# Kernel tuning notes

Measured on AMD Instinct MI355X. Metric: run time of the kernel, lower is better.

## Reference

```python
import jax, jax.numpy as jnp
import numpy as np

B, T, V, H = 128, 256, 512, 1024
EOS_ID = 1


def _onehot_seq(key, eos_pos):
    k1, = jax.random.split(key, 1)
    toks = jax.random.randint(k1, (B, T), 2, V)  # avoid 0/1 so EOS only where planted
    toks = toks.at[jnp.arange(B), eos_pos].set(EOS_ID)
    return jax.nn.one_hot(toks, V, dtype=jnp.float32)


def setup_inputs() -> dict:
    key = jax.random.key(0)
    ks = jax.random.split(key, 12)
    enc_eos = jax.random.randint(ks[0], (B,), T // 2, T)
    dec_eos = jax.random.randint(ks[1], (B,), T // 2, T)
    s = 0.05
    return {
        "encoder_inputs": _onehot_seq(ks[2], enc_eos),
        "decoder_inputs": _onehot_seq(ks[3], dec_eos),
        "enc_Wi": jax.random.normal(ks[4], (V, 4 * H), jnp.float32) * s,
        "enc_Wh": jax.random.normal(ks[5], (H, 4 * H), jnp.float32) * s,
        "enc_b": jnp.zeros((4 * H,), jnp.float32),
        "dec_Wi": jax.random.normal(ks[6], (V, 4 * H), jnp.float32) * s,
        "dec_Wh": jax.random.normal(ks[7], (H, 4 * H), jnp.float32) * s,
        "dec_b": jnp.zeros((4 * H,), jnp.float32),
        "dense_W": jax.random.normal(ks[8], (H, V), jnp.float32) * s,
        "dense_b": jnp.zeros((V,), jnp.float32),
    }


def get_sequence_lengths(seq, eos_id=EOS_ID):
    eos_row = seq[:, :, eos_id]                      # [B,T]
    eos_idx = jnp.argmax(eos_row == eos_id, axis=-1)  # first position hitting EOS
    found = eos_row[jnp.arange(seq.shape[0]), eos_idx] == eos_id
    return jnp.where(found, eos_idx + 1, seq.shape[1])


def lstm_scan(c0, h0, x_btv, Wi, Wh, b):
    """Scans an LSTM over time axis 1; returns (c_seq, h_seq) each [B,T,H]."""
    def step(carry, x):
        c, h = carry
        z = x @ Wi + h @ Wh + b                      # [B,4H]
        i, f, g, o = jnp.split(z, 4, axis=-1)
        c = jax.nn.sigmoid(f) * c + jax.nn.sigmoid(i) * jnp.tanh(g)
        h = jax.nn.sigmoid(o) * jnp.tanh(c)
        return (c, h), (c, h)
    xs = jnp.swapaxes(x_btv, 0, 1)                   # [T,B,V]
    _, (cs, hs) = jax.lax.scan(step, (c0, h0), xs)
    return jnp.swapaxes(cs, 0, 1), jnp.swapaxes(hs, 0, 1)


def reference(encoder_inputs, decoder_inputs, enc_Wi, enc_Wh, enc_b,
              dec_Wi, dec_Wh, dec_b, dense_W, dense_b):
    b = encoder_inputs.shape[0]
    # --- encoder ---
    lengths = get_sequence_lengths(encoder_inputs)
    idx = jnp.maximum(0, lengths - 1)
    c0 = jnp.zeros((b, H), encoder_inputs.dtype)
    h0 = jnp.zeros((b, H), encoder_inputs.dtype)
    cs, hs = lstm_scan(c0, h0, encoder_inputs, enc_Wi, enc_Wh, enc_b)
    ar = jnp.arange(b)
    c_enc, h_enc = cs[ar, idx], hs[ar, idx]          # carry at EOS step
    # --- decoder (teacher forcing on decoder_inputs[:, :-1]) ---
    _, hd = lstm_scan(c_enc, h_enc, decoder_inputs[:, :-1], dec_Wi, dec_Wh, dec_b)
    logits = hd @ dense_W + dense_b                  # [B,T-1,V]
    return logits
```

## Files before the change

kernel.cpp:

```cpp
#include <hip/hip_runtime.h>

#define Bv 128
#define Tv 256
#define Vv 512
#define Hv 1024
#define FH 4096
#define TD 255

typedef unsigned short ushort_t;
typedef __attribute__((ext_vector_type(8))) short bf16x8;
typedef __attribute__((ext_vector_type(4))) float f32x4;

__device__ __forceinline__ ushort_t f2bf(float f) {
    unsigned u = __float_as_uint(f);
    unsigned r = (u + 0x7fffu + ((u >> 16) & 1u)) >> 16;
    return (ushort_t)r;
}
__device__ __forceinline__ float bf2f(ushort_t h) {
    return __uint_as_float(((unsigned)h) << 16);
}
__device__ __forceinline__ float sigm(float x) {
    return 1.0f / (1.0f + expf(-x));
}

__global__ __launch_bounds__(256) void wsplit_t(
    const float* __restrict__ W, int K, int N,
    ushort_t* __restrict__ hiT, ushort_t* __restrict__ loT)
{
    __shared__ float ts[32][65];
    const int n0 = blockIdx.x * 64, k0 = blockIdx.y * 32;
    const int tid = threadIdx.x;
#pragma unroll
    for (int i = 0; i < 8; i++) {
        int f = tid + i * 256;
        int k = f >> 6, nn = f & 63;
        ts[k][nn] = W[(size_t)(k0 + k) * N + n0 + nn];
    }
    __syncthreads();
#pragma unroll
    for (int i = 0; i < 8; i++) {
        int f = tid + i * 256;
        int nn = f >> 5, k = f & 31;
        float v = ts[k][nn];
        ushort_t h = f2bf(v);
        ushort_t l = f2bf(v - bf2f(h));
        size_t o = (size_t)(n0 + nn) * K + k0 + k;
        hiT[o] = h;
        loT[o] = l;
    }
}

__global__ __launch_bounds__(256) void extract_tokens(
    const float* __restrict__ x, int* __restrict__ tok)
{
    int row = blockIdx.x * 4 + (threadIdx.x >> 6);
    int lane = threadIdx.x & 63;
    const float* p = x + (size_t)row * Vv;
    int found = -1;
#pragma unroll
    for (int i = 0; i < 8; i++)
        if (p[lane + i * 64] > 0.5f) found = lane + i * 64;
#pragma unroll
    for (int off = 32; off > 0; off >>= 1) {
        int o = __shfl_down(found, off);
        found = found > o ? found : o;
    }
    if (lane == 0) tok[row] = found;
}

__global__ void find_eos(const int* __restrict__ tok, int* __restrict__ idx)
{
    int b = threadIdx.x;
    int first = Tv - 1;
    for (int t = Tv - 1; t >= 0; t--)
        if (tok[b * Tv + t] == 1) first = t;
    idx[b] = first;
}

__global__ __launch_bounds__(256) void lstm_step(
    const ushort_t* __restrict__ WhiT, const ushort_t* __restrict__ WloT,
    const float* __restrict__ Wi,
    const float* __restrict__ bias,
    const int* __restrict__ tok, int t,
    const ushort_t* __restrict__ hin_hi, const ushort_t* __restrict__ hin_lo,
    ushort_t* __restrict__ hout_hi, ushort_t* __restrict__ hout_lo,
    float* __restrict__ c_state,
    ushort_t* __restrict__ hex_hi, ushort_t* __restrict__ hex_lo,
    const int* __restrict__ save_idx,
    float* __restrict__ c_save, ushort_t* __restrict__ hs_hi, ushort_t* __restrict__ hs_lo)
{
    __shared__ float z_s[32][68];
    const int tid = threadIdx.x;
    const int wave = tid >> 6, lane = tid & 63;
    const int wm = wave & 1, wn = wave >> 1;
    const int n = lane & 15, quad = lane >> 4;
    const int j0 = blockIdx.x * 16;
    const int b0 = blockIdx.y * 32;

    const size_t arow = (size_t)(b0 + wm * 16 + n) * Hv + quad * 8;
    const size_t g0 = (size_t)((2 * wn + 0) * Hv + j0 + n) * Hv + quad * 8;
    const size_t g1 = (size_t)((2 * wn + 1) * Hv + j0 + n) * Hv + quad * 8;

    f32x4 acc0 = {0.f, 0.f, 0.f, 0.f}, acc1 = {0.f, 0.f, 0.f, 0.f};

#pragma unroll 2
    for (int kc = 0; kc < Hv; kc += 32) {
        bf16x8 ahi = *(const bf16x8*)(hin_hi + arow + kc);
        bf16x8 alo = *(const bf16x8*)(hin_lo + arow + kc);
        bf16x8 b0h = *(const bf16x8*)(WhiT + g0 + kc);
        bf16x8 b0l = *(const bf16x8*)(WloT + g0 + kc);
        bf16x8 b1h = *(const bf16x8*)(WhiT + g1 + kc);
        bf16x8 b1l = *(const bf16x8*)(WloT + g1 + kc);
        acc0 = __builtin_amdgcn_mfma_f32_16x16x32_bf16(ahi, b0h, acc0, 0, 0, 0);
        acc1 = __builtin_amdgcn_mfma_f32_16x16x32_bf16(ahi, b1h, acc1, 0, 0, 0);
        acc0 = __builtin_amdgcn_mfma_f32_16x16x32_bf16(alo, b0h, acc0, 0, 0, 0);
        acc1 = __builtin_amdgcn_mfma_f32_16x16x32_bf16(alo, b1h, acc1, 0, 0, 0);
        acc0 = __builtin_amdgcn_mfma_f32_16x16x32_bf16(ahi, b0l, acc0, 0, 0, 0);
        acc1 = __builtin_amdgcn_mfma_f32_16x16x32_bf16(ahi, b1l, acc1, 0, 0, 0);
    }

    const int row0 = wm * 16 + quad * 4;
    const int cb0 = (2 * wn + 0) * 16 + n;
    const int cb1 = cb0 + 16;
#pragma unroll
    for (int r = 0; r < 4; r++) {
        z_s[row0 + r][cb0] = acc0[r];
        z_s[row0 + r][cb1] = acc1[r];
    }
    __syncthreads();

#pragma unroll
    for (int i = 0; i < 2; i++) {
        int p = tid + i * 256;
        int bl = p >> 4, jl = p & 15;
        int b = b0 + bl, col = j0 + jl;
        int tk = tok[b * Tv + t];
        const float* wr = Wi + (size_t)tk * FH + col;
        float zi = z_s[bl][jl]      + wr[0]        + bias[col];
        float zf = z_s[bl][16 + jl] + wr[Hv]       + bias[Hv + col];
        float zg = z_s[bl][32 + jl] + wr[2 * Hv]   + bias[2 * Hv + col];
        float zo = z_s[bl][48 + jl] + wr[3 * Hv]   + bias[3 * Hv + col];
        float si = sigm(zi), sf = sigm(zf), so = sigm(zo);
        float gg = tanhf(zg);
        size_t off = (size_t)b * Hv + col;
        float cn = sf * c_state[off] + si * gg;
        float hn = so * tanhf(cn);
        c_state[off] = cn;
        ushort_t hh = f2bf(hn);
        ushort_t hl = f2bf(hn - bf2f(hh));
        hout_hi[off] = hh;
        hout_lo[off] = hl;
        if (hex_hi) { hex_hi[off] = hh; hex_lo[off] = hl; }
        if (save_idx) {
            if (t == save_idx[b]) { c_save[off] = cn; hs_hi[off] = hh; hs_lo[off] = hl; }
        }
    }
}

__global__ __launch_bounds__(256) void dense_mfma(
    const ushort_t* __restrict__ Ahi, const ushort_t* __restrict__ Alo,
    const ushort_t* __restrict__ WhiT, const ushort_t* __restrict__ WloT,
    const float* __restrict__ bias, float* __restrict__ out)
{
    const int tid = threadIdx.x;
    const int wave = tid >> 6, lane = tid & 63;
    const int wm = wave & 1, wn = wave >> 1;
    const int n = lane & 15, quad = lane >> 4;
    const int m0 = blockIdx.y * 32 + wm * 16;
    const int c0 = blockIdx.x * 64 + wn * 32;

    const size_t arow = (size_t)(m0 + n) * Hv + quad * 8;
    const size_t g0 = (size_t)(c0 + 0 + n) * Hv + quad * 8;
    const size_t g1 = (size_t)(c0 + 16 + n) * Hv + quad * 8;

    f32x4 acc0 = {0.f, 0.f, 0.f, 0.f}, acc1 = {0.f, 0.f, 0.f, 0.f};

#pragma unroll 2
    for (int kc = 0; kc < Hv; kc += 32) {
        bf16x8 ahi = *(const bf16x8*)(Ahi + arow + kc);
        bf16x8 alo = *(const bf16x8*)(Alo + arow + kc);
        bf16x8 b0h = *(const bf16x8*)(WhiT + g0 + kc);
        bf16x8 b0l = *(const bf16x8*)(WloT + g0 + kc);
        bf16x8 b1h = *(const bf16x8*)(WhiT + g1 + kc);
        bf16x8 b1l = *(const bf16x8*)(WloT + g1 + kc);
        acc0 = __builtin_amdgcn_mfma_f32_16x16x32_bf16(ahi, b0h, acc0, 0, 0, 0);
        acc1 = __builtin_amdgcn_mfma_f32_16x16x32_bf16(ahi, b1h, acc1, 0, 0, 0);
        acc0 = __builtin_amdgcn_mfma_f32_16x16x32_bf16(alo, b0h, acc0, 0, 0, 0);
        acc1 = __builtin_amdgcn_mfma_f32_16x16x32_bf16(alo, b1h, acc1, 0, 0, 0);
        acc0 = __builtin_amdgcn_mfma_f32_16x16x32_bf16(ahi, b0l, acc0, 0, 0, 0);
        acc1 = __builtin_amdgcn_mfma_f32_16x16x32_bf16(ahi, b1l, acc1, 0, 0, 0);
    }

#pragma unroll
    for (int r = 0; r < 4; r++) {
        int row = m0 + quad * 4 + r;
        int tt = row >> 7, bb = row & 127;
        size_t o = ((size_t)bb * TD + tt) * Vv;
        int col0 = c0 + n, col1 = c0 + 16 + n;
        out[o + col0] = acc0[r] + bias[col0];
        out[o + col1] = acc1[r] + bias[col1];
    }
}

extern "C" void kernel_launch(void* const* d_in, const int* in_sizes, int n_in,
                              void* d_out, int out_size, void* d_ws, size_t ws_size,
                              hipStream_t stream)
{
    const float* enc_in  = (const float*)d_in[0];
    const float* dec_in  = (const float*)d_in[1];
    const float* enc_Wi  = (const float*)d_in[2];
    const float* enc_Wh  = (const float*)d_in[3];
    const float* enc_b   = (const float*)d_in[4];
    const float* dec_Wi  = (const float*)d_in[5];
    const float* dec_Wh  = (const float*)d_in[6];
    const float* dec_b   = (const float*)d_in[7];
    const float* dense_W = (const float*)d_in[8];
    const float* dense_b = (const float*)d_in[9];
    float* out = (float*)d_out;

    char* wp = (char*)d_ws;
    auto take = [&](size_t bytes) -> char* {
        char* p = wp;
        wp += (bytes + 255) & ~(size_t)255;
        return p;
    };

    ushort_t* hd_hi = (ushort_t*)take((size_t)TD * Bv * Hv * 2);
    ushort_t* hd_lo = (ushort_t*)take((size_t)TD * Bv * Hv * 2);
    ushort_t* eWhi  = (ushort_t*)take((size_t)FH * Hv * 2);
    ushort_t* eWlo  = (ushort_t*)take((size_t)FH * Hv * 2);
    ushort_t* dWhi  = (ushort_t*)take((size_t)FH * Hv * 2);
    ushort_t* dWlo  = (ushort_t*)take((size_t)FH * Hv * 2);
    ushort_t* nWhi  = (ushort_t*)take((size_t)Vv * Hv * 2);
    ushort_t* nWlo  = (ushort_t*)take((size_t)Vv * Hv * 2);
    ushort_t* hbh0  = (ushort_t*)take((size_t)Bv * Hv * 2);
    ushort_t* hbl0  = (ushort_t*)take((size_t)Bv * Hv * 2);
    ushort_t* hbh1  = (ushort_t*)take((size_t)Bv * Hv * 2);
    ushort_t* hbl1  = (ushort_t*)take((size_t)Bv * Hv * 2);
    ushort_t* hshi  = (ushort_t*)take((size_t)Bv * Hv * 2);
    ushort_t* hslo  = (ushort_t*)take((size_t)Bv * Hv * 2);
    float*    c_state = (float*)take((size_t)Bv * Hv * 4);
    float*    c_save  = (float*)take((size_t)Bv * Hv * 4);
    int*      etok  = (int*)take((size_t)Bv * Tv * 4);
    int*      dtok  = (int*)take((size_t)Bv * Tv * 4);
    int*      eidx  = (int*)take((size_t)Bv * 4);

    ushort_t* hbh[2] = {hbh0, hbh1};
    ushort_t* hbl[2] = {hbl0, hbl1};

    wsplit_t<<<dim3(FH / 64, Hv / 32), 256, 0, stream>>>(enc_Wh, Hv, FH, eWhi, eWlo);
    wsplit_t<<<dim3(FH / 64, Hv / 32), 256, 0, stream>>>(dec_Wh, Hv, FH, dWhi, dWlo);
    wsplit_t<<<dim3(Vv / 64, Hv / 32), 256, 0, stream>>>(dense_W, Hv, Vv, nWhi, nWlo);
    extract_tokens<<<Bv * Tv / 4, 256, 0, stream>>>(enc_in, etok);
    extract_tokens<<<Bv * Tv / 4, 256, 0, stream>>>(dec_in, dtok);
    find_eos<<<1, Bv, 0, stream>>>(etok, eidx);

    hipMemsetAsync(hbh0, 0, (size_t)Bv * Hv * 2, stream);
    hipMemsetAsync(hbl0, 0, (size_t)Bv * Hv * 2, stream);
    hipMemsetAsync(c_state, 0, (size_t)Bv * Hv * 4, stream);

    for (int t = 0; t < Tv; t++) {
        lstm_step<<<dim3(64, 4), 256, 0, stream>>>(
            eWhi, eWlo, enc_Wi, enc_b, etok, t,
            hbh[t & 1], hbl[t & 1], hbh[(t + 1) & 1], hbl[(t + 1) & 1],
            c_state, nullptr, nullptr, eidx, c_save, hshi, hslo);
    }

    hipMemcpyAsync(c_state, c_save, (size_t)Bv * Hv * 4, hipMemcpyDeviceToDevice, stream);
    hipMemcpyAsync(hbh0, hshi, (size_t)Bv * Hv * 2, hipMemcpyDeviceToDevice, stream);
    hipMemcpyAsync(hbl0, hslo, (size_t)Bv * Hv * 2, hipMemcpyDeviceToDevice, stream);

    for (int t = 0; t < TD; t++) {
        lstm_step<<<dim3(64, 4), 256, 0, stream>>>(
            dWhi, dWlo, dec_Wi, dec_b, dtok, t,
            hbh[t & 1], hbl[t & 1], hbh[(t + 1) & 1], hbl[(t + 1) & 1],
            c_state, hd_hi + (size_t)t * Bv * Hv, hd_lo + (size_t)t * Bv * Hv,
            nullptr, nullptr, nullptr, nullptr);
    }

    dense_mfma<<<dim3(Vv / 64, (TD * Bv) / 32), 256, 0, stream>>>(
        hd_hi, hd_lo, nWhi, nWlo, dense_b, out);
}
```

Baseline: 14.29 ms.

## Replace per-step LSTM launches with persistent cooperative kernel holding Wh in LDS

The 511 separate per-timestep lstm_step launches are replaced by one cooperative persistent kernel of 256 blocks. Each block keeps its 32-row slice of the recurrent weights (hi/lo bf16) resident in shared memory, keeps the cell state in registers, and separates timesteps with a grid-wide barrier. This removes per-step launch overhead and the repeated global reads of the 32 MB split weight matrices each step, and it drops the c_state round trips and device-to-device copies between encoder and decoder. In exchange every step pays a grid.sync. The kernel also depends on all 256 blocks with about 130 KB of LDS each being co-resident, which is needed for the cooperative launch to succeed.

```diff
diff --git a/kernel.cpp b/kernel.cpp
--- a/kernel.cpp
+++ b/kernel.cpp
@@ -1,4 +1,7 @@
 #include <hip/hip_runtime.h>
+#include <hip/hip_cooperative_groups.h>
+
+namespace cg = cooperative_groups;
 
 #define Bv 128
 #define Tv 256
@@ -6,6 +9,10 @@
 #define Hv 1024
 #define FH 4096
 #define TD 255
+
+#define WSTRIDE 1032
+#define W_ELEMS (32 * WSTRIDE)
+#define SMEM_BYTES (2 * W_ELEMS * 2 + 64 * 33 * 4)
 
 typedef unsigned short ushort_t;
 typedef __attribute__((ext_vector_type(8))) short bf16x8;
@@ -77,82 +84,127 @@
     idx[b] = first;
 }
 
-__global__ __launch_bounds__(256) void lstm_step(
-    const ushort_t* __restrict__ WhiT, const ushort_t* __restrict__ WloT,
-    const float* __restrict__ Wi,
-    const float* __restrict__ bias,
-    const int* __restrict__ tok, int t,
-    const ushort_t* __restrict__ hin_hi, const ushort_t* __restrict__ hin_lo,
-    ushort_t* __restrict__ hout_hi, ushort_t* __restrict__ hout_lo,
-    float* __restrict__ c_state,
-    ushort_t* __restrict__ hex_hi, ushort_t* __restrict__ hex_lo,
-    const int* __restrict__ save_idx,
-    float* __restrict__ c_save, ushort_t* __restrict__ hs_hi, ushort_t* __restrict__ hs_lo)
-{
-    __shared__ float z_s[32][68];
+struct PParams {
+    const ushort_t *eWhi, *eWlo, *dWhi, *dWlo;
+    const float *Wi_e, *b_e, *Wi_d, *b_d;
+    const int *etok, *dtok, *eidx;
+    ushort_t *h0h, *h0l, *h1h, *h1l;
+    ushort_t *hdh, *hdl;
+};
+
+__device__ __forceinline__ void load_wlds(
+    ushort_t* dst_hi, ushort_t* dst_lo,
+    const ushort_t* __restrict__ Whi, const ushort_t* __restrict__ Wlo, int j0)
+{
+    const int c = threadIdx.x >> 4, seg = threadIdx.x & 15;
+    const int grow = (c >> 3) * Hv + j0 + (c & 7);
+    const ushort_t* sh = Whi + (size_t)grow * Hv + seg * 64;
+    const ushort_t* sl = Wlo + (size_t)grow * Hv + seg * 64;
+    ushort_t* dh = dst_hi + c * WSTRIDE + seg * 64;
+    ushort_t* dl = dst_lo + c * WSTRIDE + seg * 64;
+#pragma unroll
+    for (int i = 0; i < 8; i++) {
+        *(bf16x8*)(dh + i * 8) = *(const bf16x8*)(sh + i * 8);
+        *(bf16x8*)(dl + i * 8) = *(const bf16x8*)(sl + i * 8);
+    }
+}
+
+__global__ __launch_bounds__(512, 1) void lstm_persist(PParams P)
+{
+    extern __shared__ char smem[];
+    ushort_t* Wh_hi = (ushort_t*)smem;
+    ushort_t* Wh_lo = Wh_hi + W_ELEMS;
+    float* z_s = (float*)(smem + 2 * W_ELEMS * 2);
+
+    cg::grid_group grid = cg::this_grid();
+
+    const int bid = blockIdx.x;
+    const int bg = bid & 1, cgi = bid >> 1;
+    const int b0 = bg * 64, j0 = cgi * 8;
+
     const int tid = threadIdx.x;
-    const int wave = tid >> 6, lane = tid & 63;
-    const int wm = wave & 1, wn = wave >> 1;
-    const int n = lane & 15, quad = lane >> 4;
-    const int j0 = blockIdx.x * 16;
-    const int b0 = blockIdx.y * 32;
-
-    const size_t arow = (size_t)(b0 + wm * 16 + n) * Hv + quad * 8;
-    const size_t g0 = (size_t)((2 * wn + 0) * Hv + j0 + n) * Hv + quad * 8;
-    const size_t g1 = (size_t)((2 * wn + 1) * Hv + j0 + n) * Hv + quad * 8;
-
-    f32x4 acc0 = {0.f, 0.f, 0.f, 0.f}, acc1 = {0.f, 0.f, 0.f, 0.f};
-
-#pragma unroll 2
-    for (int kc = 0; kc < Hv; kc += 32) {
-        bf16x8 ahi = *(const bf16x8*)(hin_hi + arow + kc);
-        bf16x8 alo = *(const bf16x8*)(hin_lo + arow + kc);
-        bf16x8 b0h = *(const bf16x8*)(WhiT + g0 + kc);
-        bf16x8 b0l = *(const bf16x8*)(WloT + g0 + kc);
-        bf16x8 b1h = *(const bf16x8*)(WhiT + g1 + kc);
-        bf16x8 b1l = *(const bf16x8*)(WloT + g1 + kc);
-        acc0 = __builtin_amdgcn_mfma_f32_16x16x32_bf16(ahi, b0h, acc0, 0, 0, 0);
-        acc1 = __builtin_amdgcn_mfma_f32_16x16x32_bf16(ahi, b1h, acc1, 0, 0, 0);
-        acc0 = __builtin_amdgcn_mfma_f32_16x16x32_bf16(alo, b0h, acc0, 0, 0, 0);
-        acc1 = __builtin_amdgcn_mfma_f32_16x16x32_bf16(alo, b1h, acc1, 0, 0, 0);
-        acc0 = __builtin_amdgcn_mfma_f32_16x16x32_bf16(ahi, b0l, acc0, 0, 0, 0);
-        acc1 = __builtin_amdgcn_mfma_f32_16x16x32_bf16(ahi, b1l, acc1, 0, 0, 0);
-    }
-
-    const int row0 = wm * 16 + quad * 4;
-    const int cb0 = (2 * wn + 0) * 16 + n;
-    const int cb1 = cb0 + 16;
-#pragma unroll
-    for (int r = 0; r < 4; r++) {
-        z_s[row0 + r][cb0] = acc0[r];
-        z_s[row0 + r][cb1] = acc1[r];
-    }
+    const int wv = tid >> 6, lane = tid & 63;
+    const int wm = wv & 3, wn = wv >> 2;
+    const int nn = lane & 15, quad = lane >> 4;
+
+    const size_t arow = (size_t)(b0 + wm * 16 + nn) * Hv + quad * 8;
+    const int ldsW = (wn * 16 + nn) * WSTRIDE + quad * 8;
+    const int zrow0 = wm * 16 + quad * 4;
+    const int zcol = wn * 16 + nn;
+
+    const int bl = tid >> 3, jl = tid & 7;
+    const int gb = b0 + bl;
+    const int eidx_b = P.eidx[gb];
+    const size_t ho = (size_t)gb * Hv + j0 + jl;
+    float c = 0.f, c_sav = 0.f;
+    ushort_t hs_h = 0, hs_l = 0;
+
+    load_wlds(Wh_hi, Wh_lo, P.eWhi, P.eWlo, j0);
     __syncthreads();
 
-#pragma unroll
-    for (int i = 0; i < 2; i++) {
-        int p = tid + i * 256;
-        int bl = p >> 4, jl = p & 15;
-        int b = b0 + bl, col = j0 + jl;
-        int tk = tok[b * Tv + t];
-        const float* wr = Wi + (size_t)tk * FH + col;
-        float zi = z_s[bl][jl]      + wr[0]        + bias[col];
-        float zf = z_s[bl][16 + jl] + wr[Hv]       + bias[Hv + col];
-        float zg = z_s[bl][32 + jl] + wr[2 * Hv]   + bias[2 * Hv + col];
-        float zo = z_s[bl][48 + jl] + wr[3 * Hv]   + bias[3 * Hv + col];
-        float si = sigm(zi), sf = sigm(zf), so = sigm(zo);
-        float gg = tanhf(zg);
-        size_t off = (size_t)b * Hv + col;
-        float cn = sf * c_state[off] + si * gg;
-        float hn = so * tanhf(cn);
-        c_state[off] = cn;
-        ushort_t hh = f2bf(hn);
-        ushort_t hl = f2bf(hn - bf2f(hh));
-        hout_hi[off] = hh;
-        hout_lo[off] = hl;
-        if (hex_hi) { hex_hi[off] = hh; hex_lo[off] = hl; }
-        if (save_idx) {
-            if (t == save_idx[b]) { c_save[off] = cn; hs_hi[off] = hh; hs_lo[off] = hl; }
+    for (int phase = 0; phase < 2; phase++) {
+        const int nT = phase ? TD : Tv;
+        const int* tok = phase ? P.dtok : P.etok;
+        const float* Wi = phase ? P.Wi_d : P.Wi_e;
+        const float* bias = phase ? P.b_d : P.b_e;
+
+        for (int t = 0; t < nT; t++) {
+            const ushort_t* hih = (t & 1) ? P.h1h : P.h0h;
+            const ushort_t* hil = (t & 1) ? P.h1l : P.h0l;
+            ushort_t* hoh = (t & 1) ? P.h0h : P.h1h;
+            ushort_t* hol = (t & 1) ? P.h0l : P.h1l;
+
+            f32x4 ahh = {0.f, 0.f, 0.f, 0.f};
+            f32x4 alh = {0.f, 0.f, 0.f, 0.f};
+            f32x4 ahl = {0.f, 0.f, 0.f, 0.f};
+#pragma unroll 4
+            for (int kc = 0; kc < Hv; kc += 32) {
+                bf16x8 ah = *(const bf16x8*)(hih + arow + kc);
+                bf16x8 al = *(const bf16x8*)(hil + arow + kc);
+                bf16x8 bh = *(const bf16x8*)(Wh_hi + ldsW + kc);
+                bf16x8 bl2 = *(const bf16x8*)(Wh_lo + ldsW + kc);
+                ahh = __builtin_amdgcn_mfma_f32_16x16x32_bf16(ah, bh, ahh, 0, 0, 0);
+                alh = __builtin_amdgcn_mfma_f32_16x16x32_bf16(al, bh, alh, 0, 0, 0);
+                ahl = __builtin_amdgcn_mfma_f32_16x16x32_bf16(ah, bl2, ahl, 0, 0, 0);
+            }
+#pragma unroll
+            for (int r = 0; r < 4; r++)
+                z_s[(zrow0 + r) * 33 + zcol] = ahh[r] + alh[r] + ahl[r];
+            __syncthreads();
+
+            {
+                int tk = tok[gb * Tv + t];
+                const float* wr = Wi + (size_t)tk * FH + j0 + jl;
+                const float* br = bias + j0 + jl;
+                int zb = bl * 33;
+                float zi = z_s[zb + jl]      + wr[0]        + br[0];
+                float zf = z_s[zb + 8 + jl]  + wr[Hv]       + br[Hv];
+                float zg = z_s[zb + 16 + jl] + wr[2 * Hv]   + br[2 * Hv];
+                float zo = z_s[zb + 24 + jl] + wr[3 * Hv]   + br[3 * Hv];
+                c = sigm(zf) * c + sigm(zi) * tanhf(zg);
+                float hn = sigm(zo) * tanhf(c);
+                ushort_t hh = f2bf(hn);
+                ushort_t hl = f2bf(hn - bf2f(hh));
+                hoh[ho] = hh;
+                hol[ho] = hl;
+                if (!phase) {
+                    if (t == eidx_b) { c_sav = c; hs_h = hh; hs_l = hl; }
+                } else {
+                    size_t e = (size_t)t * (Bv * Hv) + ho;
+                    P.hdh[e] = hh;
+                    P.hdl[e] = hl;
+                }
+            }
+            grid.sync();
+        }
+
+        if (!phase) {
+            load_wlds(Wh_hi, Wh_lo, P.dWhi, P.dWlo, j0);
+            c = c_sav;
+            P.h0h[ho] = hs_h;
+            P.h0l[ho] = hs_l;
+            __syncthreads();
+            grid.sync();
         }
     }
 }
@@ -237,16 +289,9 @@
     ushort_t* hbl0  = (ushort_t*)take((size_t)Bv * Hv * 2);
     ushort_t* hbh1  = (ushort_t*)take((size_t)Bv * Hv * 2);
     ushort_t* hbl1  = (ushort_t*)take((size_t)Bv * Hv * 2);
-    ushort_t* hshi  = (ushort_t*)take((size_t)Bv * Hv * 2);
-    ushort_t* hslo  = (ushort_t*)take((size_t)Bv * Hv * 2);
-    float*    c_state = (float*)take((size_t)Bv * Hv * 4);
-    float*    c_save  = (float*)take((size_t)Bv * Hv * 4);
     int*      etok  = (int*)take((size_t)Bv * Tv * 4);
     int*      dtok  = (int*)take((size_t)Bv * Tv * 4);
     int*      eidx  = (int*)take((size_t)Bv * 4);
-
-    ushort_t* hbh[2] = {hbh0, hbh1};
-    ushort_t* hbl[2] = {hbl0, hbl1};
 
     wsplit_t<<<dim3(FH / 64, Hv / 32), 256, 0, stream>>>(enc_Wh, Hv, FH, eWhi, eWlo);
     wsplit_t<<<dim3(FH / 64, Hv / 32), 256, 0, stream>>>(dec_Wh, Hv, FH, dWhi, dWlo);
@@ -257,26 +302,19 @@
 
     hipMemsetAsync(hbh0, 0, (size_t)Bv * Hv * 2, stream);
     hipMemsetAsync(hbl0, 0, (size_t)Bv * Hv * 2, stream);
-    hipMemsetAsync(c_state, 0, (size_t)Bv * Hv * 4, stream);
-
-    for (int t = 0; t < Tv; t++) {
-        lstm_step<<<dim3(64, 4), 256, 0, stream>>>(
-            eWhi, eWlo, enc_Wi, enc_b, etok, t,
-            hbh[t & 1], hbl[t & 1], hbh[(t + 1) & 1], hbl[(t + 1) & 1],
-            c_state, nullptr, nullptr, eidx, c_save, hshi, hslo);
-    }
-
-    hipMemcpyAsync(c_state, c_save, (size_t)Bv * Hv * 4, hipMemcpyDeviceToDevice, stream);
-    hipMemcpyAsync(hbh0, hshi, (size_t)Bv * Hv * 2, hipMemcpyDeviceToDevice, stream);
-    hipMemcpyAsync(hbl0, hslo, (size_t)Bv * Hv * 2, hipMemcpyDeviceToDevice, stream);
-
-    for (int t = 0; t < TD; t++) {
-        lstm_step<<<dim3(64, 4), 256, 0, stream>>>(
-            dWhi, dWlo, dec_Wi, dec_b, dtok, t,
-            hbh[t & 1], hbl[t & 1], hbh[(t + 1) & 1], hbl[(t + 1) & 1],
-            c_state, hd_hi + (size_t)t * Bv * Hv, hd_lo + (size_t)t * Bv * Hv,
-            nullptr, nullptr, nullptr, nullptr);
-    }
+
+    PParams p;
+    p.eWhi = eWhi; p.eWlo = eWlo; p.dWhi = dWhi; p.dWlo = dWlo;
+    p.Wi_e = enc_Wi; p.b_e = enc_b; p.Wi_d = dec_Wi; p.b_d = dec_b;
+    p.etok = etok; p.dtok = dtok; p.eidx = eidx;
+    p.h0h = hbh0; p.h0l = hbl0; p.h1h = hbh1; p.h1l = hbl1;
+    p.hdh = hd_hi; p.hdl = hd_lo;
+
+    hipFuncSetAttribute((const void*)lstm_persist,
+                        hipFuncAttributeMaxDynamicSharedMemorySize, SMEM_BYTES);
+    void* args[] = { &p };
+    hipLaunchCooperativeKernel((void*)lstm_persist, dim3(256), dim3(512),
+                               args, SMEM_BYTES, stream);
 
     dense_mfma<<<dim3(Vv / 64, (TD * Bv) / 32), 256, 0, stream>>>(
         hd_hi, hd_lo, nWhi, nWlo, dense_b, out);
```

New measurement: 25.21 ms. +76.4%, slower.
